# Kernel tuning notes

Measured on AMD Instinct MI355X. Metric: run time of the kernel, lower is better.

## Reference

```python
import jax, jax.numpy as jnp
import numpy as np

KERNEL = 3
PAD = 1
STRIDE = 1

def setup_inputs() -> dict:
    key = jax.random.key(0)
    k1, k2 = jax.random.split(key)
    x = jax.random.normal(k1, (32, 128, 56, 56), dtype=jnp.float32)
    # xavier_uniform-like init for weight
    fan_in = 128 * KERNEL * KERNEL
    fan_out = 256 * KERNEL * KERNEL
    limit = float(np.sqrt(6.0 / (fan_in + fan_out)))
    weight = jax.random.uniform(k2, (256, 128, KERNEL, KERNEL), dtype=jnp.float32,
                                minval=-limit, maxval=limit)
    bias = jnp.zeros((256,), dtype=jnp.float32)
    return {"x": x, "weight": weight, "bias": bias}

def reference(x, weight, bias):
    # Equivalent to the per-pixel im2col matmul loop: a standard 3x3 conv,
    # stride 1, symmetric padding 1, plus per-channel bias.
    out = jax.lax.conv_general_dilated(
        x, weight,
        window_strides=(STRIDE, STRIDE),
        padding=((PAD, PAD), (PAD, PAD)),
        dimension_numbers=("NCHW", "OIHW", "NCHW"),
    )
    return out + bias[None, :, None, None]
```

## Files before the change

kernel.cpp:

```cpp
#include <hip/hip_runtime.h>
#include <hip/hip_bf16.h>
#include <stdint.h>
#include <stddef.h>

#define NIMG 32
#define C_IN 128
#define C_OUT 256
#define HW 56
#define SP 3136
#define STOT (NIMG * SP)
#define PD 58
#define KTOT 1152

#define BM 256
#define BN 224
#define BK 64
#define NKT (KTOT / BK)
#define THREADS 512

typedef __attribute__((ext_vector_type(8))) short bf16x8;
typedef __attribute__((ext_vector_type(4))) float f32x4;

__device__ __forceinline__ void gload16(const void* g, void* l) {
    __builtin_amdgcn_global_load_lds(
        (const __attribute__((address_space(1))) void*)g,
        (__attribute__((address_space(3))) void*)l,
        16, 0, 0);
}

#define BAR() do { asm volatile("" ::: "memory"); \
                   __builtin_amdgcn_s_barrier();  \
                   asm volatile("" ::: "memory"); } while (0)
#define LGKM(n) do { asm volatile("s_waitcnt lgkmcnt(" #n ")" ::: "memory"); \
                     __builtin_amdgcn_sched_barrier(0); } while (0)
#define VMCNT(n) do { asm volatile("s_waitcnt vmcnt(" #n ")" ::: "memory"); \
                      __builtin_amdgcn_sched_barrier(0); } while (0)

__device__ __forceinline__ unsigned short bf2u(float f) {
    __hip_bfloat16 b = __float2bfloat16(f);
    return *reinterpret_cast<unsigned short*>(&b);
}

__global__ __launch_bounds__(256)
void pad_transpose_kernel(const float* __restrict__ x,
                          __hip_bfloat16* __restrict__ xp) {
    __shared__ float t[C_IN][HW + 1];
    const int hp = blockIdx.x % PD;
    const int n  = blockIdx.x / PD;
    const int h  = hp - 1;
    const bool interior = ((unsigned)h < (unsigned)HW);
    if (interior) {
        for (int idx = threadIdx.x; idx < C_IN * HW; idx += 256) {
            int ci = idx / HW, w = idx - ci * HW;
            t[ci][w] = x[((size_t)n * C_IN + ci) * SP + h * HW + w];
        }
    }
    __syncthreads();
    ushort4* dst = (ushort4*)(xp + ((size_t)n * PD + hp) * PD * C_IN);
    for (int idx = threadIdx.x; idx < PD * C_IN / 4; idx += 256) {
        int el = idx * 4;
        int wp = el >> 7, c0 = el & 127;
        ushort4 v = {0, 0, 0, 0};
        if (interior && wp >= 1 && wp <= HW) {
            int w = wp - 1;
            v.x = bf2u(t[c0 + 0][w]);
            v.y = bf2u(t[c0 + 1][w]);
            v.z = bf2u(t[c0 + 2][w]);
            v.w = bf2u(t[c0 + 3][w]);
        }
        dst[idx] = v;
    }
}

__global__ void wt_transform_kernel(const float* __restrict__ wgt,
                                    __hip_bfloat16* __restrict__ wt) {
    int idx = blockIdx.x * 256 + threadIdx.x;
    int ci  = idx & 127;
    int co  = (idx >> 7) & 255;
    int tap = idx >> 15;
    wt[idx] = __float2bfloat16(wgt[(co * C_IN + ci) * 9 + tap]);
}

__global__ __launch_bounds__(THREADS, 2)
void conv_mfma_kernel(const __hip_bfloat16* __restrict__ xp,
                      const __hip_bfloat16* __restrict__ wt,
                      const float* __restrict__ bias,
                      float* __restrict__ out) {
    extern __shared__ short smem[];

    const int tid  = threadIdx.x;
    const int lane = tid & 63;
    const int wid  = tid >> 6;
    const int wg   = (blockIdx.x & 7) * 56 + (blockIdx.x >> 3);
    const int s0   = wg * BN;

    const int cg_el = (((lane & 3) ^ ((lane >> 3) & 3)) << 3);
    const int srow  = wid * 16 + (lane >> 2);
    const int aS0   = srow * C_IN + cg_el;
    const int aS1   = aS0 + 128 * C_IN;
    int s_r = s0 + srow;
    int n_  = s_r / SP, rem = s_r - n_ * SP;
    int h_  = rem / HW, w_ = rem - h_ * HW;
    const int bS0 = ((n_ * PD + h_) * PD + w_) * C_IN + cg_el;
    int srow2 = 128 + srow; if (srow2 > BN - 1) srow2 = BN - 1;
    s_r = s0 + srow2;
    n_ = s_r / SP; rem = s_r - n_ * SP; h_ = rem / HW; w_ = rem - h_ * HW;
    const int bS1 = ((n_ * PD + h_) * PD + w_) * C_IN + cg_el;
    const int ldsw = wid * 512;

    const int rl  = lane & 15;
    const int rch = (((lane >> 4) ^ ((lane >> 1) & 3)) << 3);
    const int wm  = (wid >> 1) * 64;
    const int wn  = (wid & 1) * 112;
    const int aRd = (wm + rl) * 32 + rch;
    const int bRd = (wn + rl) * 32 + rch;

    auto STG = [&](int tau, int kk, int r) {
        int tap = tau >> 1;
        int ci0 = ((tau & 1) << 6) + (kk << 5);
        const __hip_bfloat16* wsrc = wt + tap * (C_OUT * C_IN) + ci0;
        short* Ad = smem + r * 16384 + ldsw;
        gload16(wsrc + aS0, Ad);
        gload16(wsrc + aS1, Ad + 4096);
        int kh = (tap * 11) >> 5, kw = tap - kh * 3;
        const __hip_bfloat16* xsrc = xp + (kh * PD + kw) * C_IN + ci0;
        short* Bd = smem + r * 16384 + 8192 + ldsw;
        gload16(xsrc + bS0, Bd);
        gload16(xsrc + bS1, Bd + 4096);
    };
    auto RD = [&](bf16x8* fa, bf16x8* fb, int r) {
        const short* Ab = smem + r * 16384;
        const short* Bb = Ab + 8192;
        #pragma unroll
        for (int j = 0; j < 4; ++j) fa[j] = *(const bf16x8*)(Ab + aRd + j * 512);
        #pragma unroll
        for (int j = 0; j < 7; ++j) fb[j] = *(const bf16x8*)(Bb + bRd + j * 512);
    };

    f32x4 acc[4][7] = {};
    bf16x8 fa0[4], fb0[7], fa1[4], fb1[7];

    #define MM(FA, FB) do { \
        __builtin_amdgcn_s_setprio(1); \
        _Pragma("unroll") \
        for (int mi = 0; mi < 4; ++mi) \
            _Pragma("unroll") \
            for (int ni = 0; ni < 7; ++ni) \
                acc[mi][ni] = __builtin_amdgcn_mfma_f32_16x16x32_bf16( \
                    FA[mi], FB[ni], acc[mi][ni], 0, 0, 0); \
        __builtin_amdgcn_s_setprio(0); \
    } while (0)

    STG(0, 0, 0); STG(0, 1, 1); STG(1, 0, 2);
    VMCNT(4);
    BAR();
    RD(fa0, fb0, 0);

    for (int t = 0; t < NKT; ++t) {
        const int rb = (t & 1) << 1;

        VMCNT(4);
        BAR();
        RD(fa1, fb1, rb + 1);
        if (t <= 16) STG(t + 1, 1, (rb + 3) & 3);
        LGKM(11);
        MM(fa0, fb0);

        VMCNT(4);
        BAR();
        if (t <= 16) {
            RD(fa0, fb0, (rb + 2) & 3);
            if (t <= 15) STG(t + 2, 0, rb);
            LGKM(11);
        } else {
            LGKM(0);
        }
        MM(fa1, fb1);
    }
    #undef MM

    float bv[4][4];
    #pragma unroll
    for (int mi = 0; mi < 4; ++mi)
        #pragma unroll
        for (int j = 0; j < 4; ++j)
            bv[mi][j] = bias[wm + mi * 16 + ((lane >> 4) << 2) + j];

    #pragma unroll
    for (int ni = 0; ni < 7; ++ni) {
        int s  = s0 + wn + ni * 16 + rl;
        int n  = s / SP;
        int si = s - n * SP;
        float* obase = out + (size_t)n * C_OUT * SP + si;
        #pragma unroll
        for (int mi = 0; mi < 4; ++mi) {
            int cob = wm + mi * 16 + ((lane >> 4) << 2);
            #pragma unroll
            for (int j = 0; j < 4; ++j) {
                obase[(size_t)(cob + j) * SP] = acc[mi][ni][j] + bv[mi][j];
            }
        }
    }
}

__global__ void conv_direct_kernel(const float* __restrict__ x,
                                   const float* __restrict__ wgt,
                                   const float* __restrict__ bias,
                                   float* __restrict__ out) {
    long idx = (long)blockIdx.x * 256 + threadIdx.x;
    if (idx >= (long)NIMG * C_OUT * SP) return;
    int si = (int)(idx % SP);
    int co = (int)((idx / SP) % C_OUT);
    int n  = (int)(idx / ((long)SP * C_OUT));
    int h = si / HW, w = si - (si / HW) * HW;
    float acc = bias[co];
    for (int ci = 0; ci < C_IN; ++ci) {
        const float* xr = x + ((size_t)n * C_IN + ci) * SP;
        const float* wr = wgt + ((size_t)co * C_IN + ci) * 9;
        #pragma unroll
        for (int kh = 0; kh < 3; ++kh) {
            int ih = h + kh - 1;
            if (ih < 0 || ih >= HW) continue;
            #pragma unroll
            for (int kw = 0; kw < 3; ++kw) {
                int iw = w + kw - 1;
                if (iw < 0 || iw >= HW) continue;
                acc += xr[ih * HW + iw] * wr[kh * 3 + kw];
            }
        }
    }
    out[idx] = acc;
}

extern "C" void kernel_launch(void* const* d_in, const int* in_sizes, int n_in,
                              void* d_out, int out_size, void* d_ws, size_t ws_size,
                              hipStream_t stream) {
    const float* x    = (const float*)d_in[0];
    const float* wgt  = (const float*)d_in[1];
    const float* bias = (const float*)d_in[2];
    float* out = (float*)d_out;

    const size_t xp_bytes = (size_t)NIMG * PD * PD * C_IN * sizeof(__hip_bfloat16);
    const size_t wt_bytes = (size_t)9 * C_OUT * C_IN * sizeof(__hip_bfloat16);

    if (ws_size >= xp_bytes + wt_bytes) {
        __hip_bfloat16* xp  = (__hip_bfloat16*)d_ws;
        __hip_bfloat16* wtb = (__hip_bfloat16*)((char*)d_ws + xp_bytes);

        pad_transpose_kernel<<<NIMG * PD, 256, 0, stream>>>(x, xp);
        wt_transform_kernel<<<(9 * C_OUT * C_IN) / 256, 256, 0, stream>>>(wgt, wtb);

        hipFuncSetAttribute((const void*)conv_mfma_kernel,
                            hipFuncAttributeMaxDynamicSharedMemorySize, 131072);
        conv_mfma_kernel<<<STOT / BN, THREADS, 131072, stream>>>(xp, wtb, bias, out);
    } else {
        long total = (long)NIMG * C_OUT * SP;
        conv_direct_kernel<<<(int)((total + 255) / 256), 256, 0, stream>>>(
            x, wgt, bias, out);
    }
}
```

Measured before the change: 87.88 us.

## Load weight fragments directly to registers and use a persistent tile loop

Weight (A) fragments are no longer staged through shared memory. Each wave now loads them straight from global memory into registers, which halves LDS use per stage (64KB instead of 128KB). The kernel also becomes persistent: a fixed grid of 256 blocks loops over the 448 output tiles instead of launching one block per tile. This cuts LDS traffic and footprint, but it adds per-wave redundant global loads of weights and leaves an uneven tile count per block, since 448 tiles over 256 blocks means some blocks do two tiles and some do one.

```diff
diff --git a/kernel.cpp b/kernel.cpp
--- a/kernel.cpp
+++ b/kernel.cpp
@@ -14,9 +14,10 @@
 
 #define BM 256
 #define BN 224
-#define BK 64
-#define NKT (KTOT / BK)
+#define NTILES (STOT / BN)
+#define NKT (KTOT / 64)
 #define THREADS 512
+#define GRID 256
 
 typedef __attribute__((ext_vector_type(8))) short bf16x8;
 typedef __attribute__((ext_vector_type(4))) float f32x4;
@@ -91,113 +92,117 @@
     const int tid  = threadIdx.x;
     const int lane = tid & 63;
     const int wid  = tid >> 6;
-    const int wg   = (blockIdx.x & 7) * 56 + (blockIdx.x >> 3);
-    const int s0   = wg * BN;
-
+    const int rl   = lane & 15;
+    const int kq   = lane >> 4;
+    const int wm   = (wid >> 1) * 64;
+    const int wn   = (wid & 1) * 112;
+
+    const int rch = ((kq ^ ((lane >> 1) & 3)) << 3);
+    const int bRd = (wn + rl) * 32 + rch;
     const int cg_el = (((lane & 3) ^ ((lane >> 3) & 3)) << 3);
     const int srow  = wid * 16 + (lane >> 2);
-    const int aS0   = srow * C_IN + cg_el;
-    const int aS1   = aS0 + 128 * C_IN;
-    int s_r = s0 + srow;
-    int n_  = s_r / SP, rem = s_r - n_ * SP;
-    int h_  = rem / HW, w_ = rem - h_ * HW;
-    const int bS0 = ((n_ * PD + h_) * PD + w_) * C_IN + cg_el;
-    int srow2 = 128 + srow; if (srow2 > BN - 1) srow2 = BN - 1;
-    s_r = s0 + srow2;
-    n_ = s_r / SP; rem = s_r - n_ * SP; h_ = rem / HW; w_ = rem - h_ * HW;
-    const int bS1 = ((n_ * PD + h_) * PD + w_) * C_IN + cg_el;
-    const int ldsw = wid * 512;
-
-    const int rl  = lane & 15;
-    const int rch = (((lane >> 4) ^ ((lane >> 1) & 3)) << 3);
-    const int wm  = (wid >> 1) * 64;
-    const int wn  = (wid & 1) * 112;
-    const int aRd = (wm + rl) * 32 + rch;
-    const int bRd = (wn + rl) * 32 + rch;
-
-    auto STG = [&](int tau, int kk, int r) {
-        int tap = tau >> 1;
-        int ci0 = ((tau & 1) << 6) + (kk << 5);
-        const __hip_bfloat16* wsrc = wt + tap * (C_OUT * C_IN) + ci0;
-        short* Ad = smem + r * 16384 + ldsw;
-        gload16(wsrc + aS0, Ad);
-        gload16(wsrc + aS1, Ad + 4096);
-        int kh = (tap * 11) >> 5, kw = tap - kh * 3;
-        const __hip_bfloat16* xsrc = xp + (kh * PD + kw) * C_IN + ci0;
-        short* Bd = smem + r * 16384 + 8192 + ldsw;
-        gload16(xsrc + bS0, Bd);
-        gload16(xsrc + bS1, Bd + 4096);
-    };
-    auto RD = [&](bf16x8* fa, bf16x8* fb, int r) {
-        const short* Ab = smem + r * 16384;
-        const short* Bb = Ab + 8192;
-        #pragma unroll
-        for (int j = 0; j < 4; ++j) fa[j] = *(const bf16x8*)(Ab + aRd + j * 512);
-        #pragma unroll
-        for (int j = 0; j < 7; ++j) fb[j] = *(const bf16x8*)(Bb + bRd + j * 512);
-    };
-
-    f32x4 acc[4][7] = {};
-    bf16x8 fa0[4], fb0[7], fa1[4], fb1[7];
-
-    #define MM(FA, FB) do { \
-        __builtin_amdgcn_s_setprio(1); \
-        _Pragma("unroll") \
-        for (int mi = 0; mi < 4; ++mi) \
-            _Pragma("unroll") \
-            for (int ni = 0; ni < 7; ++ni) \
-                acc[mi][ni] = __builtin_amdgcn_mfma_f32_16x16x32_bf16( \
-                    FA[mi], FB[ni], acc[mi][ni], 0, 0, 0); \
-        __builtin_amdgcn_s_setprio(0); \
-    } while (0)
-
-    STG(0, 0, 0); STG(0, 1, 1); STG(1, 0, 2);
-    VMCNT(4);
-    BAR();
-    RD(fa0, fb0, 0);
-
-    for (int t = 0; t < NKT; ++t) {
-        const int rb = (t & 1) << 1;
-
-        VMCNT(4);
-        BAR();
-        RD(fa1, fb1, rb + 1);
-        if (t <= 16) STG(t + 1, 1, (rb + 3) & 3);
-        LGKM(11);
-        MM(fa0, fb0);
-
-        VMCNT(4);
-        BAR();
-        if (t <= 16) {
-            RD(fa0, fb0, (rb + 2) & 3);
-            if (t <= 15) STG(t + 2, 0, rb);
-            LGKM(11);
-        } else {
-            LGKM(0);
-        }
-        MM(fa1, fb1);
-    }
-    #undef MM
+    const int ldsw  = wid * 512;
+    const __hip_bfloat16* Abase = wt + (wm + rl) * C_IN + kq * 8;
 
     float bv[4][4];
     #pragma unroll
     for (int mi = 0; mi < 4; ++mi)
         #pragma unroll
         for (int j = 0; j < 4; ++j)
-            bv[mi][j] = bias[wm + mi * 16 + ((lane >> 4) << 2) + j];
-
-    #pragma unroll
-    for (int ni = 0; ni < 7; ++ni) {
-        int s  = s0 + wn + ni * 16 + rl;
-        int n  = s / SP;
-        int si = s - n * SP;
-        float* obase = out + (size_t)n * C_OUT * SP + si;
+            bv[mi][j] = bias[wm + mi * 16 + (kq << 2) + j];
+
+    for (int tile = blockIdx.x; tile < NTILES; tile += GRID) {
+        const int wg = (tile & 7) * 56 + (tile >> 3);
+        const int s0 = wg * BN;
+
+        int s_r = s0 + srow;
+        int n_  = s_r / SP, rem = s_r - n_ * SP;
+        int h_  = rem / HW, w_ = rem - h_ * HW;
+        const int bS0 = ((n_ * PD + h_) * PD + w_) * C_IN + cg_el;
+        int srow2 = 128 + srow; if (srow2 > BN - 1) srow2 = BN - 1;
+        s_r = s0 + srow2;
+        n_ = s_r / SP; rem = s_r - n_ * SP; h_ = rem / HW; w_ = rem - h_ * HW;
+        const int bS1 = ((n_ * PD + h_) * PD + w_) * C_IN + cg_el;
+
+        auto STG = [&](int s, int r) {
+            int tap = s >> 2, ci0 = (s & 3) << 5;
+            int kh = (tap * 11) >> 5, kw = tap - kh * 3;
+            const __hip_bfloat16* src = xp + (kh * PD + kw) * C_IN + ci0;
+            short* d = smem + r * 8192 + ldsw;
+            gload16(src + bS0, d);
+            gload16(src + bS1, d + 4096);
+        };
+        auto LDA = [&](bf16x8* ga, int s) {
+            const __hip_bfloat16* src = Abase + ((s >> 2) << 15) + ((s & 3) << 5);
+            #pragma unroll
+            for (int mi = 0; mi < 4; ++mi)
+                ga[mi] = *(const bf16x8*)(src + mi * 16 * C_IN);
+        };
+        auto RD = [&](bf16x8* fb, int r) {
+            const short* Bb = smem + r * 8192;
+            #pragma unroll
+            for (int j = 0; j < 7; ++j)
+                fb[j] = *(const bf16x8*)(Bb + bRd + j * 512);
+        };
+
+        f32x4 acc[4][7] = {};
+        bf16x8 ga0[4], ga1[4], fb0[7], fb1[7];
+
+        #define MM(GA, FB) do { \
+            __builtin_amdgcn_s_setprio(1); \
+            _Pragma("unroll") \
+            for (int mi = 0; mi < 4; ++mi) \
+                _Pragma("unroll") \
+                for (int ni = 0; ni < 7; ++ni) \
+                    acc[mi][ni] = __builtin_amdgcn_mfma_f32_16x16x32_bf16( \
+                        GA[mi], FB[ni], acc[mi][ni], 0, 0, 0); \
+            __builtin_amdgcn_s_setprio(0); \
+        } while (0)
+
+        LDA(ga0, 0);
+        STG(0, 0); STG(1, 1); STG(2, 2);
+        VMCNT(2);
+        BAR();
+        RD(fb0, 0);
+
+        for (int t = 0; t < NKT; ++t) {
+            const int rb = (t & 1) << 1;
+
+            BAR();
+            RD(fb1, rb + 1);
+            LDA(ga1, 2 * t + 1);
+            if (t <= 16) { STG(2 * t + 3, (rb + 3) & 3); VMCNT(6); }
+            else          { VMCNT(4); }
+            LGKM(7);
+            MM(ga0, fb0);
+
+            BAR();
+            if (t <= 16) {
+                RD(fb0, (rb + 2) & 3);
+                LDA(ga0, 2 * t + 2);
+                if (t <= 15) { STG(2 * t + 4, rb); VMCNT(6); }
+                else          { VMCNT(4); }
+                LGKM(7);
+            } else {
+                VMCNT(0); LGKM(0);
+            }
+            MM(ga1, fb1);
+        }
+        #undef MM
+
         #pragma unroll
-        for (int mi = 0; mi < 4; ++mi) {
-            int cob = wm + mi * 16 + ((lane >> 4) << 2);
-            #pragma unroll
-            for (int j = 0; j < 4; ++j) {
-                obase[(size_t)(cob + j) * SP] = acc[mi][ni][j] + bv[mi][j];
+        for (int ni = 0; ni < 7; ++ni) {
+            int s  = s0 + wn + ni * 16 + rl;
+            int n  = s / SP;
+            int si = s - n * SP;
+            float* obase = out + (size_t)n * C_OUT * SP + si;
+            #pragma unroll
+            for (int mi = 0; mi < 4; ++mi) {
+                int cob = wm + mi * 16 + (kq << 2);
+                #pragma unroll
+                for (int j = 0; j < 4; ++j) {
+                    obase[(size_t)(cob + j) * SP] = acc[mi][ni][j] + bv[mi][j];
+                }
             }
         }
     }
@@ -251,8 +256,8 @@
         wt_transform_kernel<<<(9 * C_OUT * C_IN) / 256, 256, 0, stream>>>(wgt, wtb);
 
         hipFuncSetAttribute((const void*)conv_mfma_kernel,
-                            hipFuncAttributeMaxDynamicSharedMemorySize, 131072);
-        conv_mfma_kernel<<<STOT / BN, THREADS, 131072, stream>>>(xp, wtb, bias, out);
+                            hipFuncAttributeMaxDynamicSharedMemorySize, 65536);
+        conv_mfma_kernel<<<GRID, THREADS, 65536, stream>>>(xp, wtb, bias, out);
     } else {
         long total = (long)NIMG * C_OUT * SP;
         conv_direct_kernel<<<(int)((total + 255) / 256), 256, 0, stream>>>(
```

New measurement: 142.4 us. +62.0%, slower.

## Make conv kernel persistent over two tiles and fuse prep kernels

Applied to the files above, without the earlier changes.

The conv grid shrinks from 448 blocks to 224, and each block processes two output tiles in sequence. The first K-slices of the next tile are prefetched during the current tile's main loop, so pipeline fill overlaps with compute and the epilogue stores. The padding/transpose and weight-transform kernels are merged into one launch to save a kernel launch. The cost is a serialized per-block epilogue between tiles and possibly lower occupancy on 256 CUs, since 224 blocks at 2 per CU leave some CUs idle.

```diff
diff --git a/kernel.cpp b/kernel.cpp
--- a/kernel.cpp
+++ b/kernel.cpp
@@ -14,9 +14,10 @@
 
 #define BM 256
 #define BN 224
-#define BK 64
-#define NKT (KTOT / BK)
+#define NTILES (STOT / BN)
+#define NSLICE 36
 #define THREADS 512
+#define GRID 224
 
 typedef __attribute__((ext_vector_type(8))) short bf16x8;
 typedef __attribute__((ext_vector_type(4))) float f32x4;
@@ -41,44 +42,47 @@
     return *reinterpret_cast<unsigned short*>(&b);
 }
 
+#define PAD_BLOCKS (NIMG * PD)
+#define WT_BLOCKS  ((9 * C_OUT * C_IN) / 256)
+
 __global__ __launch_bounds__(256)
-void pad_transpose_kernel(const float* __restrict__ x,
-                          __hip_bfloat16* __restrict__ xp) {
+void prep_kernel(const float* __restrict__ x, const float* __restrict__ wgt,
+                 __hip_bfloat16* __restrict__ xp, __hip_bfloat16* __restrict__ wt) {
     __shared__ float t[C_IN][HW + 1];
-    const int hp = blockIdx.x % PD;
-    const int n  = blockIdx.x / PD;
-    const int h  = hp - 1;
-    const bool interior = ((unsigned)h < (unsigned)HW);
-    if (interior) {
-        for (int idx = threadIdx.x; idx < C_IN * HW; idx += 256) {
-            int ci = idx / HW, w = idx - ci * HW;
-            t[ci][w] = x[((size_t)n * C_IN + ci) * SP + h * HW + w];
-        }
-    }
-    __syncthreads();
-    ushort4* dst = (ushort4*)(xp + ((size_t)n * PD + hp) * PD * C_IN);
-    for (int idx = threadIdx.x; idx < PD * C_IN / 4; idx += 256) {
-        int el = idx * 4;
-        int wp = el >> 7, c0 = el & 127;
-        ushort4 v = {0, 0, 0, 0};
-        if (interior && wp >= 1 && wp <= HW) {
-            int w = wp - 1;
-            v.x = bf2u(t[c0 + 0][w]);
-            v.y = bf2u(t[c0 + 1][w]);
-            v.z = bf2u(t[c0 + 2][w]);
-            v.w = bf2u(t[c0 + 3][w]);
-        }
-        dst[idx] = v;
-    }
-}
-
-__global__ void wt_transform_kernel(const float* __restrict__ wgt,
-                                    __hip_bfloat16* __restrict__ wt) {
-    int idx = blockIdx.x * 256 + threadIdx.x;
-    int ci  = idx & 127;
-    int co  = (idx >> 7) & 255;
-    int tap = idx >> 15;
-    wt[idx] = __float2bfloat16(wgt[(co * C_IN + ci) * 9 + tap]);
+    const int b = blockIdx.x;
+    if (b < PAD_BLOCKS) {
+        const int hp = b % PD;
+        const int n  = b / PD;
+        const int h  = hp - 1;
+        const bool interior = ((unsigned)h < (unsigned)HW);
+        if (interior) {
+            for (int idx = threadIdx.x; idx < C_IN * HW; idx += 256) {
+                int ci = idx / HW, w = idx - ci * HW;
+                t[ci][w] = x[((size_t)n * C_IN + ci) * SP + h * HW + w];
+            }
+        }
+        __syncthreads();
+        ushort4* dst = (ushort4*)(xp + ((size_t)n * PD + hp) * PD * C_IN);
+        for (int idx = threadIdx.x; idx < PD * C_IN / 4; idx += 256) {
+            int el = idx * 4;
+            int wp = el >> 7, c0 = el & 127;
+            ushort4 v = {0, 0, 0, 0};
+            if (interior && wp >= 1 && wp <= HW) {
+                int w = wp - 1;
+                v.x = bf2u(t[c0 + 0][w]);
+                v.y = bf2u(t[c0 + 1][w]);
+                v.z = bf2u(t[c0 + 2][w]);
+                v.w = bf2u(t[c0 + 3][w]);
+            }
+            dst[idx] = v;
+        }
+    } else {
+        int idx = (b - PAD_BLOCKS) * 256 + threadIdx.x;
+        int ci  = idx & 127;
+        int co  = (idx >> 7) & 255;
+        int tap = idx >> 15;
+        wt[idx] = __float2bfloat16(wgt[(co * C_IN + ci) * 9 + tap]);
+    }
 }
 
 __global__ __launch_bounds__(THREADS, 2)
@@ -91,33 +95,40 @@
     const int tid  = threadIdx.x;
     const int lane = tid & 63;
     const int wid  = tid >> 6;
-    const int wg   = (blockIdx.x & 7) * 56 + (blockIdx.x >> 3);
-    const int s0   = wg * BN;
+    const int rl   = lane & 15;
+    const int kq   = lane >> 4;
 
     const int cg_el = (((lane & 3) ^ ((lane >> 3) & 3)) << 3);
     const int srow  = wid * 16 + (lane >> 2);
     const int aS0   = srow * C_IN + cg_el;
     const int aS1   = aS0 + 128 * C_IN;
-    int s_r = s0 + srow;
-    int n_  = s_r / SP, rem = s_r - n_ * SP;
-    int h_  = rem / HW, w_ = rem - h_ * HW;
-    const int bS0 = ((n_ * PD + h_) * PD + w_) * C_IN + cg_el;
-    int srow2 = 128 + srow; if (srow2 > BN - 1) srow2 = BN - 1;
-    s_r = s0 + srow2;
-    n_ = s_r / SP; rem = s_r - n_ * SP; h_ = rem / HW; w_ = rem - h_ * HW;
-    const int bS1 = ((n_ * PD + h_) * PD + w_) * C_IN + cg_el;
-    const int ldsw = wid * 512;
-
-    const int rl  = lane & 15;
-    const int rch = (((lane >> 4) ^ ((lane >> 1) & 3)) << 3);
+    const int ldsw  = wid * 512;
+
+    const int rch = ((kq ^ ((lane >> 1) & 3)) << 3);
     const int wm  = (wid >> 1) * 64;
     const int wn  = (wid & 1) * 112;
     const int aRd = (wm + rl) * 32 + rch;
     const int bRd = (wn + rl) * 32 + rch;
 
-    auto STG = [&](int tau, int kk, int r) {
-        int tap = tau >> 1;
-        int ci0 = ((tau & 1) << 6) + (kk << 5);
+    int ts0[2], tB0[2], tB1[2];
+    #pragma unroll
+    for (int it = 0; it < 2; ++it) {
+        int tile = blockIdx.x + it * GRID;
+        int wg   = (tile & 7) * 56 + (tile >> 3);
+        int s0   = wg * BN;
+        ts0[it]  = s0;
+        int s_r = s0 + srow;
+        int n_  = s_r / SP, rem = s_r - n_ * SP;
+        int h_  = rem / HW, w_ = rem - h_ * HW;
+        tB0[it] = ((n_ * PD + h_) * PD + w_) * C_IN + cg_el;
+        int srow2 = 128 + srow; if (srow2 > BN - 1) srow2 = BN - 1;
+        s_r = s0 + srow2;
+        n_ = s_r / SP; rem = s_r - n_ * SP; h_ = rem / HW; w_ = rem - h_ * HW;
+        tB1[it] = ((n_ * PD + h_) * PD + w_) * C_IN + cg_el;
+    }
+
+    auto STGx = [&](int sa, int r, int b0, int b1) {
+        int tap = sa >> 2, ci0 = (sa & 3) << 5;
         const __hip_bfloat16* wsrc = wt + tap * (C_OUT * C_IN) + ci0;
         short* Ad = smem + r * 16384 + ldsw;
         gload16(wsrc + aS0, Ad);
@@ -125,8 +136,8 @@
         int kh = (tap * 11) >> 5, kw = tap - kh * 3;
         const __hip_bfloat16* xsrc = xp + (kh * PD + kw) * C_IN + ci0;
         short* Bd = smem + r * 16384 + 8192 + ldsw;
-        gload16(xsrc + bS0, Bd);
-        gload16(xsrc + bS1, Bd + 4096);
+        gload16(xsrc + b0, Bd);
+        gload16(xsrc + b1, Bd + 4096);
     };
     auto RD = [&](bf16x8* fa, bf16x8* fb, int r) {
         const short* Ab = smem + r * 16384;
@@ -137,7 +148,13 @@
         for (int j = 0; j < 7; ++j) fb[j] = *(const bf16x8*)(Bb + bRd + j * 512);
     };
 
-    f32x4 acc[4][7] = {};
+    float bv[4][4];
+    #pragma unroll
+    for (int mi = 0; mi < 4; ++mi)
+        #pragma unroll
+        for (int j = 0; j < 4; ++j)
+            bv[mi][j] = bias[wm + mi * 16 + (kq << 2) + j];
+
     bf16x8 fa0[4], fb0[7], fa1[4], fb1[7];
 
     #define MM(FA, FB) do { \
@@ -151,56 +168,74 @@
         __builtin_amdgcn_s_setprio(0); \
     } while (0)
 
-    STG(0, 0, 0); STG(0, 1, 1); STG(1, 0, 2);
+    STGx(0, 0, tB0[0], tB1[0]);
+    STGx(1, 1, tB0[0], tB1[0]);
+    STGx(2, 2, tB0[0], tB1[0]);
     VMCNT(4);
     BAR();
     RD(fa0, fb0, 0);
 
-    for (int t = 0; t < NKT; ++t) {
-        const int rb = (t & 1) << 1;
-
-        VMCNT(4);
-        BAR();
-        RD(fa1, fb1, rb + 1);
-        if (t <= 16) STG(t + 1, 1, (rb + 3) & 3);
-        LGKM(11);
-        MM(fa0, fb0);
-
-        VMCNT(4);
-        BAR();
-        if (t <= 16) {
-            RD(fa0, fb0, (rb + 2) & 3);
-            if (t <= 15) STG(t + 2, 0, rb);
+    #pragma unroll
+    for (int it = 0; it < 2; ++it) {
+        const bool last = (it == 1);
+        const int cB0 = tB0[it], cB1 = tB1[it];
+        const int nB0 = tB0[it ^ 1], nB1 = tB1[it ^ 1];
+
+        f32x4 acc[4][7] = {};
+
+        #pragma unroll 1
+        for (int t = 0; t < 18; ++t) {
+            if (last && t == 17) { VMCNT(0); } else { VMCNT(4); }
+            BAR();
+            RD(fa1, fb1, (2 * t + 1) & 3);
+            {
+                int s = 2 * t + 3;
+                if (!last || s <= 35) {
+                    bool nx = s >= NSLICE;
+                    STGx(nx ? s - NSLICE : s, s & 3,
+                         nx ? nB0 : cB0, nx ? nB1 : cB1);
+                }
+            }
             LGKM(11);
-        } else {
-            LGKM(0);
-        }
-        MM(fa1, fb1);
+            MM(fa0, fb0);
+
+            VMCNT(4);
+            BAR();
+            const bool doRD = !(last && t == 17);
+            if (doRD) {
+                RD(fa0, fb0, (2 * t + 2) & 3);
+                int s = 2 * t + 4;
+                if (!last || s <= 35) {
+                    bool nx = s >= NSLICE;
+                    STGx(nx ? s - NSLICE : s, s & 3,
+                         nx ? nB0 : cB0, nx ? nB1 : cB1);
+                }
+                LGKM(11);
+            } else {
+                VMCNT(0); LGKM(0);
+            }
+            MM(fa1, fb1);
+        }
+
+        const int s0 = ts0[it];
+        #pragma unroll
+        for (int ni = 0; ni < 7; ++ni) {
+            int s  = s0 + wn + ni * 16 + rl;
+            int n  = s / SP;
+            int si = s - n * SP;
+            float* obase = out + (size_t)n * C_OUT * SP + si;
+            #pragma unroll
+            for (int mi = 0; mi < 4; ++mi) {
+                int cob = wm + mi * 16 + (kq << 2);
+                #pragma unroll
+                for (int j = 0; j < 4; ++j) {
+                    obase[(size_t)(cob + j) * SP] = acc[mi][ni][j] + bv[mi][j];
+                }
+            }
+        }
+        if (!last) { VMCNT(0); }
     }
     #undef MM
-
-    float bv[4][4];
-    #pragma unroll
-    for (int mi = 0; mi < 4; ++mi)
-        #pragma unroll
-        for (int j = 0; j < 4; ++j)
-            bv[mi][j] = bias[wm + mi * 16 + ((lane >> 4) << 2) + j];
-
-    #pragma unroll
-    for (int ni = 0; ni < 7; ++ni) {
-        int s  = s0 + wn + ni * 16 + rl;
-        int n  = s / SP;
-        int si = s - n * SP;
-        float* obase = out + (size_t)n * C_OUT * SP + si;
-        #pragma unroll
-        for (int mi = 0; mi < 4; ++mi) {
-            int cob = wm + mi * 16 + ((lane >> 4) << 2);
-            #pragma unroll
-            for (int j = 0; j < 4; ++j) {
-                obase[(size_t)(cob + j) * SP] = acc[mi][ni][j] + bv[mi][j];
-            }
-        }
-    }
 }
 
 __global__ void conv_direct_kernel(const float* __restrict__ x,
@@ -247,12 +282,11 @@
         __hip_bfloat16* xp  = (__hip_bfloat16*)d_ws;
         __hip_bfloat16* wtb = (__hip_bfloat16*)((char*)d_ws + xp_bytes);
 
-        pad_transpose_kernel<<<NIMG * PD, 256, 0, stream>>>(x, xp);
-        wt_transform_kernel<<<(9 * C_OUT * C_IN) / 256, 256, 0, stream>>>(wgt, wtb);
+        prep_kernel<<<PAD_BLOCKS + WT_BLOCKS, 256, 0, stream>>>(x, wgt, xp, wtb);
 
         hipFuncSetAttribute((const void*)conv_mfma_kernel,
                             hipFuncAttributeMaxDynamicSharedMemorySize, 131072);
-        conv_mfma_kernel<<<STOT / BN, THREADS, 131072, stream>>>(xp, wtb, bias, out);
+        conv_mfma_kernel<<<GRID, THREADS, 131072, stream>>>(xp, wtb, bias, out);
     } else {
         long total = (long)NIMG * C_OUT * SP;
         conv_direct_kernel<<<(int)((total + 255) / 256), 256, 0, stream>>>(
```

After: 106.1 us. 1.21x slower.

## Merge prep kernels and simplify MFMA pipeline waits

Applied to the files above, without the earlier changes.

Fuses the input pad/transpose and weight transform into one prep kernel launch, saving a launch. In the conv kernel it drops the explicit lgkmcnt waits and sched_barriers, leaving the compiler to schedule the LDS reads. It also reindexes the K-slice staging by slice number and hoists the bias load ahead of the main loop. The risk is that compiler-inserted waits can serialize LDS reads with the MFMAs, and the rewritten final-iteration and prologue vmcnt handling could change the overlap.

```diff
diff --git a/kernel.cpp b/kernel.cpp
--- a/kernel.cpp
+++ b/kernel.cpp
@@ -14,8 +14,7 @@
 
 #define BM 256
 #define BN 224
-#define BK 64
-#define NKT (KTOT / BK)
+#define NSLICE 36
 #define THREADS 512
 
 typedef __attribute__((ext_vector_type(8))) short bf16x8;
@@ -31,54 +30,54 @@
 #define BAR() do { asm volatile("" ::: "memory"); \
                    __builtin_amdgcn_s_barrier();  \
                    asm volatile("" ::: "memory"); } while (0)
-#define LGKM(n) do { asm volatile("s_waitcnt lgkmcnt(" #n ")" ::: "memory"); \
-                     __builtin_amdgcn_sched_barrier(0); } while (0)
-#define VMCNT(n) do { asm volatile("s_waitcnt vmcnt(" #n ")" ::: "memory"); \
-                      __builtin_amdgcn_sched_barrier(0); } while (0)
+#define VMCNT(n) asm volatile("s_waitcnt vmcnt(" #n ")" ::: "memory")
 
 __device__ __forceinline__ unsigned short bf2u(float f) {
     __hip_bfloat16 b = __float2bfloat16(f);
     return *reinterpret_cast<unsigned short*>(&b);
 }
 
+#define PAD_BLOCKS (NIMG * PD)
+#define WT_BLOCKS  ((9 * C_OUT * C_IN) / 256)
+
 __global__ __launch_bounds__(256)
-void pad_transpose_kernel(const float* __restrict__ x,
-                          __hip_bfloat16* __restrict__ xp) {
+void prep_kernel(const float* __restrict__ x, const float* __restrict__ wgt,
+                 __hip_bfloat16* __restrict__ xp, __hip_bfloat16* __restrict__ wt) {
     __shared__ float t[C_IN][HW + 1];
-    const int hp = blockIdx.x % PD;
-    const int n  = blockIdx.x / PD;
-    const int h  = hp - 1;
-    const bool interior = ((unsigned)h < (unsigned)HW);
-    if (interior) {
-        for (int idx = threadIdx.x; idx < C_IN * HW; idx += 256) {
-            int ci = idx / HW, w = idx - ci * HW;
-            t[ci][w] = x[((size_t)n * C_IN + ci) * SP + h * HW + w];
-        }
-    }
-    __syncthreads();
-    ushort4* dst = (ushort4*)(xp + ((size_t)n * PD + hp) * PD * C_IN);
-    for (int idx = threadIdx.x; idx < PD * C_IN / 4; idx += 256) {
-        int el = idx * 4;
-        int wp = el >> 7, c0 = el & 127;
-        ushort4 v = {0, 0, 0, 0};
-        if (interior && wp >= 1 && wp <= HW) {
-            int w = wp - 1;
-            v.x = bf2u(t[c0 + 0][w]);
-            v.y = bf2u(t[c0 + 1][w]);
-            v.z = bf2u(t[c0 + 2][w]);
-            v.w = bf2u(t[c0 + 3][w]);
-        }
-        dst[idx] = v;
-    }
-}
-
-__global__ void wt_transform_kernel(const float* __restrict__ wgt,
-                                    __hip_bfloat16* __restrict__ wt) {
-    int idx = blockIdx.x * 256 + threadIdx.x;
-    int ci  = idx & 127;
-    int co  = (idx >> 7) & 255;
-    int tap = idx >> 15;
-    wt[idx] = __float2bfloat16(wgt[(co * C_IN + ci) * 9 + tap]);
+    const int b = blockIdx.x;
+    if (b < PAD_BLOCKS) {
+        const int hp = b % PD;
+        const int n  = b / PD;
+        const int h  = hp - 1;
+        const bool interior = ((unsigned)h < (unsigned)HW);
+        if (interior) {
+            for (int idx = threadIdx.x; idx < C_IN * HW; idx += 256) {
+                int ci = idx / HW, w = idx - ci * HW;
+                t[ci][w] = x[((size_t)n * C_IN + ci) * SP + h * HW + w];
+            }
+        }
+        __syncthreads();
+        ushort4* dst = (ushort4*)(xp + ((size_t)n * PD + hp) * PD * C_IN);
+        for (int idx = threadIdx.x; idx < PD * C_IN / 4; idx += 256) {
+            int el = idx * 4;
+            int wp = el >> 7, c0 = el & 127;
+            ushort4 v = {0, 0, 0, 0};
+            if (interior && wp >= 1 && wp <= HW) {
+                int w = wp - 1;
+                v.x = bf2u(t[c0 + 0][w]);
+                v.y = bf2u(t[c0 + 1][w]);
+                v.z = bf2u(t[c0 + 2][w]);
+                v.w = bf2u(t[c0 + 3][w]);
+            }
+            dst[idx] = v;
+        }
+    } else {
+        int idx = (b - PAD_BLOCKS) * 256 + threadIdx.x;
+        int ci  = idx & 127;
+        int co  = (idx >> 7) & 255;
+        int tap = idx >> 15;
+        wt[idx] = __float2bfloat16(wgt[(co * C_IN + ci) * 9 + tap]);
+    }
 }
 
 __global__ __launch_bounds__(THREADS, 2)
@@ -91,6 +90,8 @@
     const int tid  = threadIdx.x;
     const int lane = tid & 63;
     const int wid  = tid >> 6;
+    const int rl   = lane & 15;
+    const int kq   = lane >> 4;
     const int wg   = (blockIdx.x & 7) * 56 + (blockIdx.x >> 3);
     const int s0   = wg * BN;
 
@@ -98,6 +99,7 @@
     const int srow  = wid * 16 + (lane >> 2);
     const int aS0   = srow * C_IN + cg_el;
     const int aS1   = aS0 + 128 * C_IN;
+    const int ldsw  = wid * 512;
     int s_r = s0 + srow;
     int n_  = s_r / SP, rem = s_r - n_ * SP;
     int h_  = rem / HW, w_ = rem - h_ * HW;
@@ -106,25 +108,22 @@
     s_r = s0 + srow2;
     n_ = s_r / SP; rem = s_r - n_ * SP; h_ = rem / HW; w_ = rem - h_ * HW;
     const int bS1 = ((n_ * PD + h_) * PD + w_) * C_IN + cg_el;
-    const int ldsw = wid * 512;
-
-    const int rl  = lane & 15;
-    const int rch = (((lane >> 4) ^ ((lane >> 1) & 3)) << 3);
+
+    const int rch = ((kq ^ ((lane >> 1) & 3)) << 3);
     const int wm  = (wid >> 1) * 64;
     const int wn  = (wid & 1) * 112;
     const int aRd = (wm + rl) * 32 + rch;
     const int bRd = (wn + rl) * 32 + rch;
 
-    auto STG = [&](int tau, int kk, int r) {
-        int tap = tau >> 1;
-        int ci0 = ((tau & 1) << 6) + (kk << 5);
+    auto STG = [&](int s) {
+        int tap = s >> 2, ci0 = (s & 3) << 5;
         const __hip_bfloat16* wsrc = wt + tap * (C_OUT * C_IN) + ci0;
-        short* Ad = smem + r * 16384 + ldsw;
+        short* Ad = smem + (s & 3) * 16384 + ldsw;
         gload16(wsrc + aS0, Ad);
         gload16(wsrc + aS1, Ad + 4096);
         int kh = (tap * 11) >> 5, kw = tap - kh * 3;
         const __hip_bfloat16* xsrc = xp + (kh * PD + kw) * C_IN + ci0;
-        short* Bd = smem + r * 16384 + 8192 + ldsw;
+        short* Bd = smem + (s & 3) * 16384 + 8192 + ldsw;
         gload16(xsrc + bS0, Bd);
         gload16(xsrc + bS1, Bd + 4096);
     };
@@ -136,6 +135,13 @@
         #pragma unroll
         for (int j = 0; j < 7; ++j) fb[j] = *(const bf16x8*)(Bb + bRd + j * 512);
     };
+
+    float bv[4][4];
+    #pragma unroll
+    for (int mi = 0; mi < 4; ++mi)
+        #pragma unroll
+        for (int j = 0; j < 4; ++j)
+            bv[mi][j] = bias[wm + mi * 16 + (kq << 2) + j];
 
     f32x4 acc[4][7] = {};
     bf16x8 fa0[4], fb0[7], fa1[4], fb1[7];
@@ -151,40 +157,30 @@
         __builtin_amdgcn_s_setprio(0); \
     } while (0)
 
-    STG(0, 0, 0); STG(0, 1, 1); STG(1, 0, 2);
-    VMCNT(4);
+    STG(0); STG(1); STG(2);
+    VMCNT(8);
     BAR();
     RD(fa0, fb0, 0);
 
-    for (int t = 0; t < NKT; ++t) {
-        const int rb = (t & 1) << 1;
-
-        VMCNT(4);
+    for (int t = 0; t < 18; ++t) {
+        if (t == 17) { VMCNT(0); } else { VMCNT(4); }
         BAR();
-        RD(fa1, fb1, rb + 1);
-        if (t <= 16) STG(t + 1, 1, (rb + 3) & 3);
-        LGKM(11);
+        RD(fa1, fb1, (2 * t + 1) & 3);
+        if (t <= 16) STG(2 * t + 3);
         MM(fa0, fb0);
 
-        VMCNT(4);
-        BAR();
-        if (t <= 16) {
-            RD(fa0, fb0, (rb + 2) & 3);
-            if (t <= 15) STG(t + 2, 0, rb);
-            LGKM(11);
+        if (t < 17) {
+            VMCNT(4);
+            BAR();
+            RD(fa0, fb0, (2 * t + 2) & 3);
+            if (t <= 15) STG(2 * t + 4);
+            MM(fa1, fb1);
         } else {
-            LGKM(0);
-        }
-        MM(fa1, fb1);
+            BAR();
+            MM(fa1, fb1);
+        }
     }
     #undef MM
-
-    float bv[4][4];
-    #pragma unroll
-    for (int mi = 0; mi < 4; ++mi)
-        #pragma unroll
-        for (int j = 0; j < 4; ++j)
-            bv[mi][j] = bias[wm + mi * 16 + ((lane >> 4) << 2) + j];
 
     #pragma unroll
     for (int ni = 0; ni < 7; ++ni) {
@@ -194,7 +190,7 @@
         float* obase = out + (size_t)n * C_OUT * SP + si;
         #pragma unroll
         for (int mi = 0; mi < 4; ++mi) {
-            int cob = wm + mi * 16 + ((lane >> 4) << 2);
+            int cob = wm + mi * 16 + (kq << 2);
             #pragma unroll
             for (int j = 0; j < 4; ++j) {
                 obase[(size_t)(cob + j) * SP] = acc[mi][ni][j] + bv[mi][j];
@@ -247,8 +243,7 @@
         __hip_bfloat16* xp  = (__hip_bfloat16*)d_ws;
         __hip_bfloat16* wtb = (__hip_bfloat16*)((char*)d_ws + xp_bytes);
 
-        pad_transpose_kernel<<<NIMG * PD, 256, 0, stream>>>(x, xp);
-        wt_transform_kernel<<<(9 * C_OUT * C_IN) / 256, 256, 0, stream>>>(wgt, wtb);
+        prep_kernel<<<PAD_BLOCKS + WT_BLOCKS, 256, 0, stream>>>(x, wgt, xp, wtb);
 
         hipFuncSetAttribute((const void*)conv_mfma_kernel,
                             hipFuncAttributeMaxDynamicSharedMemorySize, 131072);
```

Result: faster. 84.99 us, median of 2 (-3.3%).
